# Performance work log

Measured on AMD Instinct MI355X. Metric: run time of the kernel, lower is better.

## Reference

```python
import jax, jax.numpy as jnp
import numpy as np

jax.config.update("jax_enable_x64", True)

DIM = 128          # state dimension
T = 4096           # number of time points
BATCH = 64         # batched initial conditions (columns of x0)
N_UPPER = DIM * (DIM - 1) // 2  # 8128


def setup_inputs() -> dict:
    key = jax.random.key(0)
    k1, k2 = jax.random.split(key)
    return {
        "t": jnp.arange(T, dtype=jnp.float64) * 0.01,               # uniform time grid
        "x0": jax.random.normal(k1, (DIM, BATCH), dtype=jnp.float64),
        "S_upper": jax.random.normal(k2, (N_UPPER,), dtype=jnp.float64) * 0.3,
        "D_raw": jnp.ones((DIM,), dtype=jnp.float64) * 0.1,
    }


def _get_A(S_upper, D_raw):
    # skew-symmetric S from upper-triangular entries, minus positive diagonal D
    iu, ju = np.triu_indices(DIM, k=1)  # static index sets
    S = jnp.zeros((DIM, DIM), dtype=S_upper.dtype).at[iu, ju].set(S_upper)
    S = S - S.T
    return S - jnp.diag(jax.nn.softplus(D_raw))


def reference(t, x0, S_upper, D_raw):
    A = _get_A(S_upper, D_raw)
    dt = t[1] - t[0]
    expAdt = jax.scipy.linalg.expm(A * dt)  # [DIM, DIM]

    def step(x, _):
        x = expAdt @ x  # [DIM, BATCH]
        return x, x

    _, ys = jax.lax.scan(step, x0, None, length=T - 1)  # [T-1, DIM, BATCH]
    return jnp.concatenate([x0[None], ys], axis=0)      # [T, DIM, BATCH]
```

## Files before the change

kernel.cpp:

```cpp
#include <hip/hip_runtime.h>
#include <math.h>

#define DIM 128
#define GP(s)    ((s) * 16384)
#define YOFFI    (65 * 16384)
#define XOFF(q)  ((97 + (q)) * 16384)
#define TOFF(i)  ((105 + (i) - 1) * 16384)
#define FWOFFI   (169 * 16384)
#define FYOFFI   (201 * 16384)

typedef _Float16 f16x8 __attribute__((ext_vector_type(8)));
typedef float    f32x4 __attribute__((ext_vector_type(4)));

__device__ __forceinline__ float4 ld4(const float* p) { return *(const float4*)p; }

__device__ __forceinline__ void stageA(const float* __restrict__ A, float* AT, int tid)
{
    for (int idx = tid; idx < DIM * DIM; idx += 256)
        AT[(idx & 127) * 132 + (idx >> 7)] = A[idx];
}

__device__ __forceinline__ void mm_core(const float* AT, const float* Bs,
                                        float (&acc)[4][4], int tid)
{
    int d0 = (tid & 31) * 4, c0 = (tid >> 5) * 4;
    #pragma unroll 4
    for (int k = 0; k < DIM; k++) {
        float4 a4 = ld4(&AT[k * 132 + d0]);
        float4 b4 = ld4(&Bs[k * 36 + c0]);
        float a_[4] = {a4.x, a4.y, a4.z, a4.w};
        float b_[4] = {b4.x, b4.y, b4.z, b4.w};
        #pragma unroll
        for (int i = 0; i < 4; i++)
            #pragma unroll
            for (int j = 0; j < 4; j++) acc[i][j] += a_[i] * b_[j];
    }
}

__device__ __forceinline__ void mm_plain(const float* __restrict__ A,
                                         const float* __restrict__ B,
                                         float* __restrict__ C,
                                         int ncols, int cpan,
                                         float* AT, float* Bs, int tid)
{
    stageA(A, AT, tid);
    for (int idx = tid; idx < DIM * 32; idx += 256) {
        int k = idx >> 5, cc = idx & 31;
        Bs[k * 36 + cc] = B[(size_t)k * ncols + cpan + cc];
    }
    __syncthreads();
    float acc[4][4] = {};
    mm_core(AT, Bs, acc, tid);
    int d0 = (tid & 31) * 4, c0 = (tid >> 5) * 4;
    #pragma unroll
    for (int i = 0; i < 4; i++) {
        float4 st = make_float4(acc[i][0], acc[i][1], acc[i][2], acc[i][3]);
        *(float4*)&C[(size_t)(d0 + i) * ncols + cpan + c0] = st;
    }
}

__global__ __launch_bounds__(256) void k_x2(const float* __restrict__ t,
                                            const float* __restrict__ x0,
                                            const float* __restrict__ S,
                                            const float* __restrict__ D,
                                            float* __restrict__ ws)
{
    __shared__ __align__(16) float AT[DIM * 132];
    __shared__ __align__(16) float Bs[DIM * 36];
    int tid = threadIdx.x, bid = blockIdx.x, cpan = bid * 32;
    float dt = t[1] - t[0];
    for (int e = tid; e < 16384; e += 256) {
        int r = e >> 7, c = e & 127;
        float a;
        if (r == c)      a = -log1pf(expf(D[r]));
        else if (r < c)  a =  S[(r * (2 * DIM - r - 1)) / 2 + (c - r - 1)];
        else             a = -S[(c * (2 * DIM - c - 1)) / 2 + (r - c - 1)];
        a *= dt;
        AT[c * 132 + r] = a;
        if (c >= cpan && c < cpan + 32) Bs[r * 36 + (c - cpan)] = a;
        if (bid == 0) ws[XOFF(0) + e] = a;
    }
    if (bid == 1) for (int e = tid; e < 8192; e += 256) ws[YOFFI + e] = x0[e];
    if (bid == 2) {
        _Float16* Wf = (_Float16*)(ws + FWOFFI);
        for (int ch = tid; ch < 2048; ch += 256) {
            int m = ch >> 4, k0 = (ch & 15) << 3;
            f16x8 hv;
            #pragma unroll
            for (int q = 0; q < 8; q++) hv[q] = (m == k0 + q) ? (_Float16)1.0f : (_Float16)0.0f;
            int lane = (m & 15) | (((k0 >> 3) & 3) << 4);
            size_t off = (((size_t)(m >> 4) * 4 + (k0 >> 5)) * 64 + lane) * 8;
            *(f16x8*)(Wf + off) = hv;
        }
    }
    __syncthreads();
    float acc[4][4] = {};
    mm_core(AT, Bs, acc, tid);
    int d0 = (tid & 31) * 4, c0 = (tid >> 5) * 4;
    #pragma unroll
    for (int r = 0; r < 4; r++) {
        float4 st = make_float4(acc[r][0], acc[r][1], acc[r][2], acc[r][3]);
        *(float4*)&ws[XOFF(1) + (size_t)(d0 + r) * DIM + cpan + c0] = st;
    }
}

struct Jobs { int4 jb[16]; };

__global__ __launch_bounds__(256) void k_lvl(float* __restrict__ ws, Jobs jobs)
{
    __shared__ __align__(16) float AT[DIM * 132];
    __shared__ __align__(16) float Bs[DIM * 36];
    int4 jb = jobs.jb[blockIdx.x];
    int ncols = jb.w;
    int cpan = blockIdx.y * 32;
    if (cpan >= ncols) return;
    mm_plain(ws + jb.x, ws + jb.y, ws + jb.z, ncols, cpan, AT, Bs, threadIdx.x);
}

__global__ __launch_bounds__(256) void k_ps1(float* __restrict__ ws)
{
    __shared__ __align__(16) float AT[DIM * 132];
    __shared__ __align__(16) float Bs[DIM * 36];
    int i = blockIdx.x + 1, cpan = blockIdx.y * 32, tid = threadIdx.x;
    float c[24]; c[0] = 1.0f;
    #pragma unroll
    for (int n = 1; n < 24; n++) c[n] = c[n - 1] * ((float)i / (float)n);
    stageA(ws + XOFF(7), AT, tid);
    for (int idx = tid; idx < DIM * 8; idx += 256) {
        int k = idx >> 3, cc4 = (idx & 7) * 4;
        float4 b = make_float4(0.f, 0.f, 0.f, 0.f);
        #pragma unroll
        for (int q = 1; q < 8; q++) {
            float4 x = ld4(&ws[XOFF(q - 1) + (size_t)k * DIM + cpan + cc4]);
            b.x += c[16 + q] * x.x; b.y += c[16 + q] * x.y;
            b.z += c[16 + q] * x.z; b.w += c[16 + q] * x.w;
        }
        int col = cpan + cc4;
        if (k >= col && k < col + 4) (&b.x)[k - col] += c[16];
        *(float4*)&Bs[k * 36 + cc4] = b;
    }
    __syncthreads();
    float acc[4][4] = {};
    mm_core(AT, Bs, acc, tid);
    int d0 = (tid & 31) * 4, c0 = (tid >> 5) * 4;
    float* T = ws + TOFF(i);
    #pragma unroll
    for (int r = 0; r < 4; r++) {
        int dd = d0 + r;
        float add[4] = {0.f, 0.f, 0.f, 0.f};
        #pragma unroll
        for (int q = 1; q < 8; q++) {
            float4 x = ld4(&ws[XOFF(q - 1) + (size_t)dd * DIM + cpan + c0]);
            add[0] += c[8 + q] * x.x; add[1] += c[8 + q] * x.y;
            add[2] += c[8 + q] * x.z; add[3] += c[8 + q] * x.w;
        }
        int col0 = cpan + c0;
        if (dd >= col0 && dd < col0 + 4) add[dd - col0] += c[8];
        float4 st = make_float4(acc[r][0] + add[0], acc[r][1] + add[1],
                                acc[r][2] + add[2], acc[r][3] + add[3]);
        *(float4*)&T[(size_t)dd * DIM + cpan + c0] = st;
    }
}

__global__ __launch_bounds__(256) void k_ps2(float* __restrict__ ws)
{
    __shared__ __align__(16) float AT[DIM * 132];
    __shared__ __align__(16) float Bs[DIM * 36];
    int i = blockIdx.x + 1, cpan = blockIdx.y * 32, tid = threadIdx.x;
    float c[8]; c[0] = 1.0f;
    #pragma unroll
    for (int n = 1; n < 8; n++) c[n] = c[n - 1] * ((float)i / (float)n);
    stageA(ws + XOFF(7), AT, tid);
    const float* T = ws + TOFF(i);
    for (int idx = tid; idx < DIM * 32; idx += 256) {
        int k = idx >> 5, cc = idx & 31;
        Bs[k * 36 + cc] = T[(size_t)k * DIM + cpan + cc];
    }
    __syncthreads();
    float acc[4][4] = {};
    mm_core(AT, Bs, acc, tid);
    int d0 = (tid & 31) * 4, c0 = (tid >> 5) * 4;
    #pragma unroll
    for (int r = 0; r < 4; r++) {
        int dd = d0 + r;
        float add[4] = {0.f, 0.f, 0.f, 0.f};
        #pragma unroll
        for (int q = 1; q < 8; q++) {
            float4 x = ld4(&ws[XOFF(q - 1) + (size_t)dd * DIM + cpan + c0]);
            add[0] += c[q] * x.x; add[1] += c[q] * x.y;
            add[2] += c[q] * x.z; add[3] += c[q] * x.w;
        }
        int col0 = cpan + c0;
        if (dd >= col0 && dd < col0 + 4) add[dd - col0] += 1.0f;
        #pragma unroll
        for (int j = 0; j < 4; j++) acc[r][j] += add[j];
    }
    if (i == 64) {
        float* G = ws + GP(0);
        #pragma unroll
        for (int r = 0; r < 4; r++) {
            float4 st = make_float4(acc[r][0], acc[r][1], acc[r][2], acc[r][3]);
            *(float4*)&G[(size_t)(d0 + r) * DIM + cpan + c0] = st;
        }
        return;
    }
    __syncthreads();
    #pragma unroll
    for (int r = 0; r < 4; r++)
        #pragma unroll
        for (int j = 0; j < 4; j++) Bs[(d0 + r) * 36 + c0 + j] = acc[r][j];
    __syncthreads();
    _Float16* Wf = (_Float16*)(ws + FWOFFI);
    for (int ch = tid; ch < 512; ch += 256) {
        int m = ch >> 2, k0l = (ch & 3) * 8, k0 = cpan + k0l;
        f16x8 hv;
        #pragma unroll
        for (int q = 0; q < 8; q++) hv[q] = (_Float16)Bs[m * 36 + k0l + q];
        int lane = (m & 15) | (((k0 >> 3) & 3) << 4);
        size_t off = (size_t)i * 16384 + (((size_t)(m >> 4) * 4 + (k0 >> 5)) * 64 + lane) * 8;
        *(f16x8*)(Wf + off) = hv;
    }
}

__global__ __launch_bounds__(256) void k_ylev(float* __restrict__ ws, int gslot,
                                              int jbase, int njobs,
                                              int nconvmats, int write_f32,
                                              int sq_from, int sq_to)
{
    __shared__ __align__(16) float AT[DIM * 132];
    __shared__ __align__(16) float Bs[DIM * 36];
    int bid = blockIdx.x, tid = threadIdx.x;
    int ncomp = njobs * 2;
    int nconvw = nconvmats * 4;
    _Float16* Yf = (_Float16*)(ws + FYOFFI);
    if (bid < ncomp) {
        int jj = bid >> 1, bc = (bid & 1) * 32;
        int jout = jbase + jj;
        stageA(ws + GP(gslot), AT, tid);
        for (int idx = tid; idx < DIM * 32; idx += 256) {
            int k = idx >> 5, cc = idx & 31;
            Bs[k * 36 + cc] = ws[YOFFI + (size_t)jj * 8192 + (size_t)k * 64 + bc + cc];
        }
        __syncthreads();
        float acc[4][4] = {};
        mm_core(AT, Bs, acc, tid);
        int d0 = (tid & 31) * 4, c0 = (tid >> 5) * 4;
        __syncthreads();
        if (write_f32) {
            #pragma unroll
            for (int r = 0; r < 4; r++) {
                float4 st = make_float4(acc[r][0], acc[r][1], acc[r][2], acc[r][3]);
                *(float4*)&ws[YOFFI + (size_t)jout * 8192 + (size_t)(d0 + r) * 64 + bc + c0] = st;
            }
        }
        #pragma unroll
        for (int r = 0; r < 4; r++)
            #pragma unroll
            for (int j = 0; j < 4; j++) Bs[(d0 + r) * 36 + c0 + j] = acc[r][j];
        __syncthreads();
        for (int ch = tid; ch < 512; ch += 256) {
            int nloc = ch >> 4, k0 = (ch & 15) * 8;
            f16x8 hv;
            #pragma unroll
            for (int q = 0; q < 8; q++) hv[q] = (_Float16)Bs[(k0 + q) * 36 + nloc];
            int n = bc + nloc;
            int lane = (n & 15) | (((k0 >> 3) & 3) << 4);
            size_t off = (size_t)jout * 8192 + (((size_t)(n >> 4) * 4 + (k0 >> 5)) * 64 + lane) * 8;
            *(f16x8*)(Yf + off) = hv;
        }
    } else if (bid < ncomp + nconvw) {
        int g = (bid - ncomp) * 256 + tid;
        int j = g >> 10, cidx = g & 1023;
        int n = cidx >> 4, k0 = (cidx & 15) << 3;
        const float* src = ws + YOFFI + (size_t)j * 8192 + n;
        f16x8 hv;
        #pragma unroll
        for (int q = 0; q < 8; q++) hv[q] = (_Float16)src[(size_t)(k0 + q) * 64];
        int lane = (n & 15) | (((k0 >> 3) & 3) << 4);
        size_t off = (size_t)j * 8192 + (((size_t)(n >> 4) * 4 + (k0 >> 5)) * 64 + lane) * 8;
        *(f16x8*)(Yf + off) = hv;
    } else {
        int pan = (bid - ncomp - nconvw) * 32;
        mm_plain(ws + GP(sq_from), ws + GP(sq_from), ws + GP(sq_to), 128, pan, AT, Bs, tid);
    }
}

__global__ __launch_bounds__(256) void k_final(const _Float16* __restrict__ Wf,
                                               const _Float16* __restrict__ Yf,
                                               float* __restrict__ out)
{
    int i = blockIdx.x, j = blockIdx.y;
    int tid = threadIdx.x, wave = tid >> 6, lane = tid & 63;
    const _Float16* Ab = Yf + (size_t)j * 8192;
    const _Float16* Bb = Wf + (size_t)i * 16384;
    f32x4 acc[4][2] = {};
    #pragma unroll
    for (int ks = 0; ks < 4; ks++) {
        f16x8 a[4], b[2];
        #pragma unroll
        for (int bt = 0; bt < 4; bt++)
            a[bt] = *(const f16x8*)(Ab + (((size_t)bt * 4 + ks) * 64 + lane) * 8);
        #pragma unroll
        for (int nn = 0; nn < 2; nn++)
            b[nn] = *(const f16x8*)(Bb + (((size_t)(wave * 2 + nn) * 4 + ks) * 64 + lane) * 8);
        #pragma unroll
        for (int bt = 0; bt < 4; bt++)
            #pragma unroll
            for (int nn = 0; nn < 2; nn++)
                acc[bt][nn] = __builtin_amdgcn_mfma_f32_16x16x32_f16(a[bt], b[nn], acc[bt][nn], 0, 0, 0);
    }
    float* slab = out + (size_t)(j * 64 + i) * 8192;
    int nlo = lane & 15, b0 = (lane >> 4) * 4;
    #pragma unroll
    for (int bt = 0; bt < 4; bt++)
        #pragma unroll
        for (int nn = 0; nn < 2; nn++) {
            int n = (wave * 2 + nn) * 16 + nlo;
            __builtin_nontemporal_store(acc[bt][nn],
                (f32x4*)&slab[(size_t)n * 64 + bt * 16 + b0]);
        }
}

static inline void addjob(Jobs& J, int& n, int a, int b, int c, int nc)
{
    J.jb[n++] = make_int4(a, b, c, nc);
}

extern "C" void kernel_launch(void* const* d_in, const int* in_sizes, int n_in,
                              void* d_out, int out_size, void* d_ws, size_t ws_size,
                              hipStream_t stream)
{
    const float* t  = (const float*)d_in[0];
    const float* x0 = (const float*)d_in[1];
    const float* S  = (const float*)d_in[2];
    const float* D  = (const float*)d_in[3];
    float* out = (float*)d_out;
    float* ws  = (float*)d_ws;
    _Float16* Wf = (_Float16*)(ws + FWOFFI);
    _Float16* Yf = (_Float16*)(ws + FYOFFI);

    hipLaunchKernelGGL(k_x2, dim3(4), dim3(256), 0, stream, t, x0, S, D, ws);

    Jobs J; int n;
    n = 0;
    addjob(J, n, XOFF(1), XOFF(0), XOFF(2), 128);
    addjob(J, n, XOFF(1), XOFF(1), XOFF(3), 128);
    hipLaunchKernelGGL(k_lvl, dim3(n, 4), dim3(256), 0, stream, ws, J);
    n = 0;
    for (int q = 1; q <= 4; q++) addjob(J, n, XOFF(3), XOFF(q - 1), XOFF(3 + q), 128);
    hipLaunchKernelGGL(k_lvl, dim3(n, 4), dim3(256), 0, stream, ws, J);

    hipLaunchKernelGGL(k_ps1, dim3(64, 4), dim3(256), 0, stream, ws);
    hipLaunchKernelGGL(k_ps2, dim3(64, 4), dim3(256), 0, stream, ws);

    n = 0;
    addjob(J, n, GP(0), GP(0), GP(1), 128);
    addjob(J, n, GP(0), YOFFI, YOFFI + 8192, 64);
    hipLaunchKernelGGL(k_lvl, dim3(n, 4), dim3(256), 0, stream, ws, J);
    n = 0;
    addjob(J, n, GP(1), GP(1), GP(2), 128);
    addjob(J, n, GP(1), YOFFI,        YOFFI + 2 * 8192, 64);
    addjob(J, n, GP(1), YOFFI + 8192, YOFFI + 3 * 8192, 64);
    hipLaunchKernelGGL(k_lvl, dim3(n, 4), dim3(256), 0, stream, ws, J);
    n = 0;
    addjob(J, n, GP(2), GP(2), GP(3), 128);
    for (int jj = 0; jj < 4; jj++)
        addjob(J, n, GP(2), YOFFI + jj * 8192, YOFFI + (4 + jj) * 8192, 64);
    hipLaunchKernelGGL(k_lvl, dim3(n, 4), dim3(256), 0, stream, ws, J);
    n = 0;
    addjob(J, n, GP(3), GP(3), GP(4), 128);
    for (int jj = 0; jj < 8; jj++)
        addjob(J, n, GP(3), YOFFI + jj * 8192, YOFFI + (8 + jj) * 8192, 64);
    hipLaunchKernelGGL(k_lvl, dim3(n, 4), dim3(256), 0, stream, ws, J);

    hipLaunchKernelGGL(k_ylev, dim3(36), dim3(256), 0, stream, ws, 4, 16, 16, 0, 1, 4, 5);
    hipLaunchKernelGGL(k_ylev, dim3(128), dim3(256), 0, stream, ws, 5, 32, 32, 16, 0, -1, -1);

    hipLaunchKernelGGL(k_final, dim3(64, 64), dim3(256), 0, stream, Wf, Yf, out);
}
```

Baseline: 213.8 us.

## Replace FP32 level matmuls with split-FP16 MFMA kernel and scaled Taylor basis

Replaces the SIMT fp32 panel matmul (k_lvl/k_ylev) with a single-block-per-job k_mm that computes full 128xN products on MFMA units, using hi/lo fp16 splitting (three MFMAs) to keep near-fp32 accuracy. It fuses the fp16 fragment conversion of Y into the matmul epilogue, so the separate conversion blocks go away. It also scales A*dt by 16 and adjusts the Taylor coefficients to match. The change trades four panel blocks per job for one larger block, which lowers parallelism, and the split-fp16 arithmetic may lose some precision.

Result: slower. 218.1 us (+2.0%).

```diff
diff --git a/kernel.cpp b/kernel.cpp
--- a/kernel.cpp
+++ b/kernel.cpp
@@ -8,6 +8,7 @@
 #define TOFF(i)  ((105 + (i) - 1) * 16384)
 #define FWOFFI   (169 * 16384)
 #define FYOFFI   (201 * 16384)
+#define ALPHA    16.0f
 
 typedef _Float16 f16x8 __attribute__((ext_vector_type(8)));
 typedef float    f32x4 __attribute__((ext_vector_type(4)));
@@ -37,28 +38,6 @@
     }
 }
 
-__device__ __forceinline__ void mm_plain(const float* __restrict__ A,
-                                         const float* __restrict__ B,
-                                         float* __restrict__ C,
-                                         int ncols, int cpan,
-                                         float* AT, float* Bs, int tid)
-{
-    stageA(A, AT, tid);
-    for (int idx = tid; idx < DIM * 32; idx += 256) {
-        int k = idx >> 5, cc = idx & 31;
-        Bs[k * 36 + cc] = B[(size_t)k * ncols + cpan + cc];
-    }
-    __syncthreads();
-    float acc[4][4] = {};
-    mm_core(AT, Bs, acc, tid);
-    int d0 = (tid & 31) * 4, c0 = (tid >> 5) * 4;
-    #pragma unroll
-    for (int i = 0; i < 4; i++) {
-        float4 st = make_float4(acc[i][0], acc[i][1], acc[i][2], acc[i][3]);
-        *(float4*)&C[(size_t)(d0 + i) * ncols + cpan + c0] = st;
-    }
-}
-
 __global__ __launch_bounds__(256) void k_x2(const float* __restrict__ t,
                                             const float* __restrict__ x0,
                                             const float* __restrict__ S,
@@ -68,14 +47,14 @@
     __shared__ __align__(16) float AT[DIM * 132];
     __shared__ __align__(16) float Bs[DIM * 36];
     int tid = threadIdx.x, bid = blockIdx.x, cpan = bid * 32;
-    float dt = t[1] - t[0];
+    float sc = (t[1] - t[0]) * ALPHA;
     for (int e = tid; e < 16384; e += 256) {
         int r = e >> 7, c = e & 127;
         float a;
         if (r == c)      a = -log1pf(expf(D[r]));
         else if (r < c)  a =  S[(r * (2 * DIM - r - 1)) / 2 + (c - r - 1)];
         else             a = -S[(c * (2 * DIM - c - 1)) / 2 + (r - c - 1)];
-        a *= dt;
+        a *= sc;
         AT[c * 132 + r] = a;
         if (c >= cpan && c < cpan + 32) Bs[r * 36 + (c - cpan)] = a;
         if (bid == 0) ws[XOFF(0) + e] = a;
@@ -93,6 +72,18 @@
             *(f16x8*)(Wf + off) = hv;
         }
     }
+    if (bid == 3) {
+        _Float16* Yf = (_Float16*)(ws + FYOFFI);
+        for (int slot = tid; slot < 1024; slot += 256) {
+            int ls = slot & 63, tile = slot >> 6;
+            int n = (tile >> 2) * 16 + (ls & 15);
+            int k0 = (tile & 3) * 32 + ((ls >> 4) & 3) * 8;
+            f16x8 hv;
+            #pragma unroll
+            for (int q = 0; q < 8; q++) hv[q] = (_Float16)x0[(size_t)(k0 + q) * 64 + n];
+            *(f16x8*)(Yf + (size_t)slot * 8) = hv;
+        }
+    }
     __syncthreads();
     float acc[4][4] = {};
     mm_core(AT, Bs, acc, tid);
@@ -104,17 +95,101 @@
     }
 }
 
-struct Jobs { int4 jb[16]; };
-
-__global__ __launch_bounds__(256) void k_lvl(float* __restrict__ ws, Jobs jobs)
-{
-    __shared__ __align__(16) float AT[DIM * 132];
-    __shared__ __align__(16) float Bs[DIM * 36];
-    int4 jb = jobs.jb[blockIdx.x];
-    int ncols = jb.w;
-    int cpan = blockIdx.y * 32;
-    if (cpan >= ncols) return;
-    mm_plain(ws + jb.x, ws + jb.y, ws + jb.z, ncols, cpan, AT, Bs, threadIdx.x);
+struct Jobs { int4 jb[33]; };
+
+__global__ __launch_bounds__(256) void k_mm(float* __restrict__ ws, Jobs jobs)
+{
+    __shared__ __align__(16) _Float16 fB[2][16384];
+    const int4 jb = jobs.jb[blockIdx.x];
+    const int ncols = jb.w & 255;
+    const int fragj = (jb.w >> 8) - 1;
+    const float* A = ws + jb.x;
+    const float* B = ws + jb.y;
+    float* C = ws + jb.z;
+    const int tid = threadIdx.x, wave = tid >> 6, lane = tid & 63;
+
+    f16x8 ah[2][4], al[2][4];
+    #pragma unroll
+    for (int mt = 0; mt < 2; mt++)
+        #pragma unroll
+        for (int kc = 0; kc < 4; kc++) {
+            int m = wave * 32 + mt * 16 + (lane & 15);
+            int k0 = kc * 32 + ((lane >> 4) & 3) * 8;
+            const float* src = A + (size_t)m * DIM + k0;
+            float4 p = ld4(src), r = ld4(src + 4);
+            float v[8] = {p.x, p.y, p.z, p.w, r.x, r.y, r.z, r.w};
+            f16x8 h8, l8;
+            #pragma unroll
+            for (int q = 0; q < 8; q++) {
+                _Float16 h = (_Float16)v[q];
+                h8[q] = h; l8[q] = (_Float16)(v[q] - (float)h);
+            }
+            ah[mt][kc] = h8; al[mt][kc] = l8;
+        }
+
+    const int nslots = (DIM * ncols) >> 3;
+    for (int slot = tid; slot < nslots; slot += 256) {
+        int ls = slot & 63, tile = slot >> 6;
+        int n = (tile >> 2) * 16 + (ls & 15);
+        int k0 = (tile & 3) * 32 + ((ls >> 4) & 3) * 8;
+        f16x8 h8, l8;
+        #pragma unroll
+        for (int q = 0; q < 8; q++) {
+            float v = B[(size_t)(k0 + q) * ncols + n];
+            _Float16 h = (_Float16)v;
+            h8[q] = h; l8[q] = (_Float16)(v - (float)h);
+        }
+        *(f16x8*)&fB[0][(size_t)slot * 8] = h8;
+        *(f16x8*)&fB[1][(size_t)slot * 8] = l8;
+    }
+    __syncthreads();
+
+    const int NT = ncols >> 4;
+    f32x4 acc[2][8] = {};
+    for (int kc = 0; kc < 4; kc++) {
+        #pragma unroll
+        for (int nt = 0; nt < 8; nt++) {
+            if (nt >= NT) break;
+            size_t bo = ((size_t)(nt * 4 + kc) * 64 + lane) * 8;
+            f16x8 bh = *(const f16x8*)&fB[0][bo];
+            f16x8 bl = *(const f16x8*)&fB[1][bo];
+            #pragma unroll
+            for (int mt = 0; mt < 2; mt++) {
+                acc[mt][nt] = __builtin_amdgcn_mfma_f32_16x16x32_f16(ah[mt][kc], bh, acc[mt][nt], 0, 0, 0);
+                acc[mt][nt] = __builtin_amdgcn_mfma_f32_16x16x32_f16(ah[mt][kc], bl, acc[mt][nt], 0, 0, 0);
+                acc[mt][nt] = __builtin_amdgcn_mfma_f32_16x16x32_f16(al[mt][kc], bh, acc[mt][nt], 0, 0, 0);
+            }
+        }
+    }
+    __syncthreads();
+
+    float* Cst = (float*)&fB[0][0];
+    #pragma unroll
+    for (int mt = 0; mt < 2; mt++)
+        #pragma unroll
+        for (int nt = 0; nt < 8; nt++) {
+            if (nt >= NT) break;
+            int row = wave * 32 + mt * 16 + ((lane >> 4) << 2);
+            int n = nt * 16 + (lane & 15);
+            #pragma unroll
+            for (int p = 0; p < 4; p++)
+                Cst[(size_t)(row + p) * ncols + n] = acc[mt][nt][p];
+        }
+    __syncthreads();
+    for (int e = tid * 4; e < DIM * ncols; e += 1024)
+        *(float4*)&C[e] = ld4(&Cst[e]);
+    if (fragj >= 0) {
+        _Float16* Yf = (_Float16*)(ws + FYOFFI) + (size_t)fragj * 8192;
+        for (int slot = tid; slot < 1024; slot += 256) {
+            int ls = slot & 63, tile = slot >> 6;
+            int n = (tile >> 2) * 16 + (ls & 15);
+            int k0 = (tile & 3) * 32 + ((ls >> 4) & 3) * 8;
+            f16x8 hv;
+            #pragma unroll
+            for (int q = 0; q < 8; q++) hv[q] = (_Float16)Cst[(size_t)(k0 + q) * 64 + n];
+            *(f16x8*)(Yf + (size_t)slot * 8) = hv;
+        }
+    }
 }
 
 __global__ __launch_bounds__(256) void k_ps1(float* __restrict__ ws)
@@ -122,9 +197,10 @@
     __shared__ __align__(16) float AT[DIM * 132];
     __shared__ __align__(16) float Bs[DIM * 36];
     int i = blockIdx.x + 1, cpan = blockIdx.y * 32, tid = threadIdx.x;
+    float r = (float)i / ALPHA;
     float c[24]; c[0] = 1.0f;
     #pragma unroll
-    for (int n = 1; n < 24; n++) c[n] = c[n - 1] * ((float)i / (float)n);
+    for (int n = 1; n < 24; n++) c[n] = c[n - 1] * (r / (float)n);
     stageA(ws + XOFF(7), AT, tid);
     for (int idx = tid; idx < DIM * 8; idx += 256) {
         int k = idx >> 3, cc4 = (idx & 7) * 4;
@@ -145,8 +221,8 @@
     int d0 = (tid & 31) * 4, c0 = (tid >> 5) * 4;
     float* T = ws + TOFF(i);
     #pragma unroll
-    for (int r = 0; r < 4; r++) {
-        int dd = d0 + r;
+    for (int rr = 0; rr < 4; rr++) {
+        int dd = d0 + rr;
         float add[4] = {0.f, 0.f, 0.f, 0.f};
         #pragma unroll
         for (int q = 1; q < 8; q++) {
@@ -156,8 +232,8 @@
         }
         int col0 = cpan + c0;
         if (dd >= col0 && dd < col0 + 4) add[dd - col0] += c[8];
-        float4 st = make_float4(acc[r][0] + add[0], acc[r][1] + add[1],
-                                acc[r][2] + add[2], acc[r][3] + add[3]);
+        float4 st = make_float4(acc[rr][0] + add[0], acc[rr][1] + add[1],
+                                acc[rr][2] + add[2], acc[rr][3] + add[3]);
         *(float4*)&T[(size_t)dd * DIM + cpan + c0] = st;
     }
 }
@@ -167,9 +243,10 @@
     __shared__ __align__(16) float AT[DIM * 132];
     __shared__ __align__(16) float Bs[DIM * 36];
     int i = blockIdx.x + 1, cpan = blockIdx.y * 32, tid = threadIdx.x;
+    float r = (float)i / ALPHA;
     float c[8]; c[0] = 1.0f;
     #pragma unroll
-    for (int n = 1; n < 8; n++) c[n] = c[n - 1] * ((float)i / (float)n);
+    for (int n = 1; n < 8; n++) c[n] = c[n - 1] * (r / (float)n);
     stageA(ws + XOFF(7), AT, tid);
     const float* T = ws + TOFF(i);
     for (int idx = tid; idx < DIM * 32; idx += 256) {
@@ -181,8 +258,8 @@
     mm_core(AT, Bs, acc, tid);
     int d0 = (tid & 31) * 4, c0 = (tid >> 5) * 4;
     #pragma unroll
-    for (int r = 0; r < 4; r++) {
-        int dd = d0 + r;
+    for (int rr = 0; rr < 4; rr++) {
+        int dd = d0 + rr;
         float add[4] = {0.f, 0.f, 0.f, 0.f};
         #pragma unroll
         for (int q = 1; q < 8; q++) {
@@ -193,22 +270,22 @@
         int col0 = cpan + c0;
         if (dd >= col0 && dd < col0 + 4) add[dd - col0] += 1.0f;
         #pragma unroll
-        for (int j = 0; j < 4; j++) acc[r][j] += add[j];
+        for (int j = 0; j < 4; j++) acc[rr][j] += add[j];
     }
     if (i == 64) {
         float* G = ws + GP(0);
         #pragma unroll
-        for (int r = 0; r < 4; r++) {
-            float4 st = make_float4(acc[r][0], acc[r][1], acc[r][2], acc[r][3]);
-            *(float4*)&G[(size_t)(d0 + r) * DIM + cpan + c0] = st;
+        for (int rr = 0; rr < 4; rr++) {
+            float4 st = make_float4(acc[rr][0], acc[rr][1], acc[rr][2], acc[rr][3]);
+            *(float4*)&G[(size_t)(d0 + rr) * DIM + cpan + c0] = st;
         }
         return;
     }
     __syncthreads();
     #pragma unroll
-    for (int r = 0; r < 4; r++)
-        #pragma unroll
-        for (int j = 0; j < 4; j++) Bs[(d0 + r) * 36 + c0 + j] = acc[r][j];
+    for (int rr = 0; rr < 4; rr++)
+        #pragma unroll
+        for (int j = 0; j < 4; j++) Bs[(d0 + rr) * 36 + c0 + j] = acc[rr][j];
     __syncthreads();
     _Float16* Wf = (_Float16*)(ws + FWOFFI);
     for (int ch = tid; ch < 512; ch += 256) {
@@ -219,69 +296,6 @@
         int lane = (m & 15) | (((k0 >> 3) & 3) << 4);
         size_t off = (size_t)i * 16384 + (((size_t)(m >> 4) * 4 + (k0 >> 5)) * 64 + lane) * 8;
         *(f16x8*)(Wf + off) = hv;
-    }
-}
-
-__global__ __launch_bounds__(256) void k_ylev(float* __restrict__ ws, int gslot,
-                                              int jbase, int njobs,
-                                              int nconvmats, int write_f32,
-                                              int sq_from, int sq_to)
-{
-    __shared__ __align__(16) float AT[DIM * 132];
-    __shared__ __align__(16) float Bs[DIM * 36];
-    int bid = blockIdx.x, tid = threadIdx.x;
-    int ncomp = njobs * 2;
-    int nconvw = nconvmats * 4;
-    _Float16* Yf = (_Float16*)(ws + FYOFFI);
-    if (bid < ncomp) {
-        int jj = bid >> 1, bc = (bid & 1) * 32;
-        int jout = jbase + jj;
-        stageA(ws + GP(gslot), AT, tid);
-        for (int idx = tid; idx < DIM * 32; idx += 256) {
-            int k = idx >> 5, cc = idx & 31;
-            Bs[k * 36 + cc] = ws[YOFFI + (size_t)jj * 8192 + (size_t)k * 64 + bc + cc];
-        }
-        __syncthreads();
-        float acc[4][4] = {};
-        mm_core(AT, Bs, acc, tid);
-        int d0 = (tid & 31) * 4, c0 = (tid >> 5) * 4;
-        __syncthreads();
-        if (write_f32) {
-            #pragma unroll
-            for (int r = 0; r < 4; r++) {
-                float4 st = make_float4(acc[r][0], acc[r][1], acc[r][2], acc[r][3]);
-                *(float4*)&ws[YOFFI + (size_t)jout * 8192 + (size_t)(d0 + r) * 64 + bc + c0] = st;
-            }
-        }
-        #pragma unroll
-        for (int r = 0; r < 4; r++)
-            #pragma unroll
-            for (int j = 0; j < 4; j++) Bs[(d0 + r) * 36 + c0 + j] = acc[r][j];
-        __syncthreads();
-        for (int ch = tid; ch < 512; ch += 256) {
-            int nloc = ch >> 4, k0 = (ch & 15) * 8;
-            f16x8 hv;
-            #pragma unroll
-            for (int q = 0; q < 8; q++) hv[q] = (_Float16)Bs[(k0 + q) * 36 + nloc];
-            int n = bc + nloc;
-            int lane = (n & 15) | (((k0 >> 3) & 3) << 4);
-            size_t off = (size_t)jout * 8192 + (((size_t)(n >> 4) * 4 + (k0 >> 5)) * 64 + lane) * 8;
-            *(f16x8*)(Yf + off) = hv;
-        }
-    } else if (bid < ncomp + nconvw) {
-        int g = (bid - ncomp) * 256 + tid;
-        int j = g >> 10, cidx = g & 1023;
-        int n = cidx >> 4, k0 = (cidx & 15) << 3;
-        const float* src = ws + YOFFI + (size_t)j * 8192 + n;
-        f16x8 hv;
-        #pragma unroll
-        for (int q = 0; q < 8; q++) hv[q] = (_Float16)src[(size_t)(k0 + q) * 64];
-        int lane = (n & 15) | (((k0 >> 3) & 3) << 4);
-        size_t off = (size_t)j * 8192 + (((size_t)(n >> 4) * 4 + (k0 >> 5)) * 64 + lane) * 8;
-        *(f16x8*)(Yf + off) = hv;
-    } else {
-        int pan = (bid - ncomp - nconvw) * 32;
-        mm_plain(ws + GP(sq_from), ws + GP(sq_from), ws + GP(sq_to), 128, pan, AT, Bs, tid);
     }
 }
 
@@ -321,9 +335,9 @@
         }
 }
 
-static inline void addjob(Jobs& J, int& n, int a, int b, int c, int nc)
-{
-    J.jb[n++] = make_int4(a, b, c, nc);
+static inline void addjob(Jobs& J, int& n, int a, int b, int c, int ncols, int fragj)
+{
+    J.jb[n++] = make_int4(a, b, c, ncols | ((fragj + 1) << 8));
 }
 
 extern "C" void kernel_launch(void* const* d_in, const int* in_sizes, int n_in,
@@ -343,38 +357,44 @@
 
     Jobs J; int n;
     n = 0;
-    addjob(J, n, XOFF(1), XOFF(0), XOFF(2), 128);
-    addjob(J, n, XOFF(1), XOFF(1), XOFF(3), 128);
-    hipLaunchKernelGGL(k_lvl, dim3(n, 4), dim3(256), 0, stream, ws, J);
-    n = 0;
-    for (int q = 1; q <= 4; q++) addjob(J, n, XOFF(3), XOFF(q - 1), XOFF(3 + q), 128);
-    hipLaunchKernelGGL(k_lvl, dim3(n, 4), dim3(256), 0, stream, ws, J);
+    addjob(J, n, XOFF(1), XOFF(0), XOFF(2), 128, -1);
+    addjob(J, n, XOFF(1), XOFF(1), XOFF(3), 128, -1);
+    hipLaunchKernelGGL(k_mm, dim3(n), dim3(256), 0, stream, ws, J);
+    n = 0;
+    for (int q = 1; q <= 4; q++) addjob(J, n, XOFF(3), XOFF(q - 1), XOFF(3 + q), 128, -1);
+    hipLaunchKernelGGL(k_mm, dim3(n), dim3(256), 0, stream, ws, J);
 
     hipLaunchKernelGGL(k_ps1, dim3(64, 4), dim3(256), 0, stream, ws);
     hipLaunchKernelGGL(k_ps2, dim3(64, 4), dim3(256), 0, stream, ws);
 
     n = 0;
-    addjob(J, n, GP(0), GP(0), GP(1), 128);
-    addjob(J, n, GP(0), YOFFI, YOFFI + 8192, 64);
-    hipLaunchKernelGGL(k_lvl, dim3(n, 4), dim3(256), 0, stream, ws, J);
-    n = 0;
-    addjob(J, n, GP(1), GP(1), GP(2), 128);
-    addjob(J, n, GP(1), YOFFI,        YOFFI + 2 * 8192, 64);
-    addjob(J, n, GP(1), YOFFI + 8192, YOFFI + 3 * 8192, 64);
-    hipLaunchKernelGGL(k_lvl, dim3(n, 4), dim3(256), 0, stream, ws, J);
-    n = 0;
-    addjob(J, n, GP(2), GP(2), GP(3), 128);
+    addjob(J, n, GP(0), GP(0), GP(1), 128, -1);
+    addjob(J, n, GP(0), YOFFI, YOFFI + 8192, 64, 1);
+    hipLaunchKernelGGL(k_mm, dim3(n), dim3(256), 0, stream, ws, J);
+    n = 0;
+    addjob(J, n, GP(1), GP(1), GP(2), 128, -1);
+    addjob(J, n, GP(1), YOFFI,        YOFFI + 2 * 8192, 64, 2);
+    addjob(J, n, GP(1), YOFFI + 8192, YOFFI + 3 * 8192, 64, 3);
+    hipLaunchKernelGGL(k_mm, dim3(n), dim3(256), 0, stream, ws, J);
+    n = 0;
+    addjob(J, n, GP(2), GP(2), GP(3), 128, -1);
     for (int jj = 0; jj < 4; jj++)
-        addjob(J, n, GP(2), YOFFI + jj * 8192, YOFFI + (4 + jj) * 8192, 64);
-    hipLaunchKernelGGL(k_lvl, dim3(n, 4), dim3(256), 0, stream, ws, J);
-    n = 0;
-    addjob(J, n, GP(3), GP(3), GP(4), 128);
+        addjob(J, n, GP(2), YOFFI + jj * 8192, YOFFI + (4 + jj) * 8192, 64, 4 + jj);
+    hipLaunchKernelGGL(k_mm, dim3(n), dim3(256), 0, stream, ws, J);
+    n = 0;
+    addjob(J, n, GP(3), GP(3), GP(4), 128, -1);
     for (int jj = 0; jj < 8; jj++)
-        addjob(J, n, GP(3), YOFFI + jj * 8192, YOFFI + (8 + jj) * 8192, 64);
-    hipLaunchKernelGGL(k_lvl, dim3(n, 4), dim3(256), 0, stream, ws, J);
-
-    hipLaunchKernelGGL(k_ylev, dim3(36), dim3(256), 0, stream, ws, 4, 16, 16, 0, 1, 4, 5);
-    hipLaunchKernelGGL(k_ylev, dim3(128), dim3(256), 0, stream, ws, 5, 32, 32, 16, 0, -1, -1);
+        addjob(J, n, GP(3), YOFFI + jj * 8192, YOFFI + (8 + jj) * 8192, 64, 8 + jj);
+    hipLaunchKernelGGL(k_mm, dim3(n), dim3(256), 0, stream, ws, J);
+    n = 0;
+    addjob(J, n, GP(4), GP(4), GP(5), 128, -1);
+    for (int jj = 0; jj < 16; jj++)
+        addjob(J, n, GP(4), YOFFI + jj * 8192, YOFFI + (16 + jj) * 8192, 64, 16 + jj);
+    hipLaunchKernelGGL(k_mm, dim3(n), dim3(256), 0, stream, ws, J);
+    n = 0;
+    for (int jj = 0; jj < 32; jj++)
+        addjob(J, n, GP(5), YOFFI + jj * 8192, YOFFI + (32 + jj) * 8192, 64, 32 + jj);
+    hipLaunchKernelGGL(k_mm, dim3(n), dim3(256), 0, stream, ws, J);
 
     hipLaunchKernelGGL(k_final, dim3(64, 64), dim3(256), 0, stream, Wf, Yf, out);
 }
```
